# Performance work log

Measured on AMD Instinct MI355X. Metric: run time of the kernel, lower is better.

The kernel has to match this reference:

```python
import jax, jax.numpy as jnp
import numpy as np

B, T, N_EMBED, HEAD_SIZE = 8, 2048, 1024, 64


def setup_inputs() -> dict:
    key = jax.random.key(0)
    kx, kq, kk, kv = jax.random.split(key, 4)
    x = jax.random.normal(kx, (B, T, N_EMBED), dtype=jnp.float32)
    # nn.Linear(n_embed, head_size, bias=False) -> weight [head_size, n_embed];
    # we store the transposed [n_embed, head_size] so projection is x @ W.
    s = 1.0 / np.sqrt(N_EMBED)
    Wq = jax.random.normal(kq, (N_EMBED, HEAD_SIZE), dtype=jnp.float32) * s
    Wk = jax.random.normal(kk, (N_EMBED, HEAD_SIZE), dtype=jnp.float32) * s
    Wv = jax.random.normal(kv, (N_EMBED, HEAD_SIZE), dtype=jnp.float32) * s
    pad_mask = jnp.ones((B, T), dtype=jnp.int32)
    return {"x": x, "pad_mask": pad_mask, "Wq": Wq, "Wk": Wk, "Wv": Wv}


def reference(x, pad_mask, Wq, Wk, Wv):
    Bq, Tq, C = x.shape  # C == n_embed
    q = x @ Wq  # [B,T,H]
    k = x @ Wk  # self-attention path (enc_x is None)
    v = x @ Wv
    # NOTE: original divides by C**0.5 with C = n_embed, not head_size.
    scores = jnp.einsum("bth,bsh->bts", q, k) / jnp.sqrt(jnp.asarray(C, x.dtype))
    causal = jnp.tril(jnp.ones((Tq, Tq), dtype=bool))  # tril[:T,:T] != 0
    keep = causal[None, :, :] & (pad_mask[:, None, :] != 0)  # [B,T,T]
    scores = jnp.where(keep, scores, -jnp.inf)
    attn = jax.nn.softmax(scores, axis=-1)
    return jnp.einsum("bts,bsh->bth", attn, v)  # [B,T,head_size]
```

## Files before the change

### kernel.cpp

```cpp
#include <hip/hip_runtime.h>

#define DEV static __device__ __forceinline__

typedef float f32x4 __attribute__((ext_vector_type(4)));
typedef __bf16 bf16x8 __attribute__((ext_vector_type(8)));
typedef unsigned short u16x8 __attribute__((ext_vector_type(8)));
typedef unsigned short u16x4 __attribute__((ext_vector_type(4)));

#define MFMA(a, b, c) __builtin_amdgcn_mfma_f32_16x16x32_bf16((a), (b), (c), 0, 0, 0)

#define TT 2048
#define CE 1024
#define HS 64

#define WBT_E 0
#define Q_E   196608
#define K_E   (Q_E + 1048576)
#define VT_E  (K_E + 1048576)
#define PO_E  (VT_E + 1048576)
#define PML_E (PO_E + 2097152)
#define BIAS_E (PML_E + 131072)

DEV unsigned short cvt_bf16(float f) {
    unsigned int u = __builtin_bit_cast(unsigned int, f);
    u += 0x7FFFu + ((u >> 16) & 1u);
    return (unsigned short)(u >> 16);
}

DEV float bf2f(unsigned short v) {
    unsigned int u = ((unsigned int)v) << 16;
    return __builtin_bit_cast(float, u);
}

DEV bf16x8 ld_bf8(const unsigned short* p) {
    union { u16x8 u; bf16x8 b; } v;
    v.u = *(const u16x8*)p;
    return v.b;
}

DEV bf16x8 as_bf8(u16x8 u) {
    union { u16x8 u; bf16x8 b; } v;
    v.u = u;
    return v.b;
}

DEV void glds16(const void* g, void* l) {
    __builtin_amdgcn_global_load_lds(
        (const __attribute__((address_space(1))) void*)g,
        (__attribute__((address_space(3))) void*)l, 16, 0, 0);
}

__global__ __launch_bounds__(256) void wconv_kernel(
        const float* __restrict__ Wq, const float* __restrict__ Wk,
        const float* __restrict__ Wv, unsigned short* __restrict__ wbt) {
    __shared__ unsigned short Tr[64 * 72];
    const int blk = blockIdx.x;
    const int head = blk >> 4, kt = blk & 15;
    const int k0 = kt * 64;
    const float* W = (head == 0) ? Wq : ((head == 1) ? Wk : Wv);
    const float sc = (head == 0) ? 0.045084220027780106f : 1.0f;
    const int t = threadIdx.x;
    const int rrow = t >> 4, c4 = (t & 15) * 4;
    for (int i = 0; i < 4; ++i) {
        int krow = rrow + i * 16;
        f32x4 f = *(const f32x4*)(W + (size_t)(k0 + krow) * 64 + c4);
        Tr[(c4 + 0) * 72 + krow] = cvt_bf16(f[0] * sc);
        Tr[(c4 + 1) * 72 + krow] = cvt_bf16(f[1] * sc);
        Tr[(c4 + 2) * 72 + krow] = cvt_bf16(f[2] * sc);
        Tr[(c4 + 3) * 72 + krow] = cvt_bf16(f[3] * sc);
    }
    __syncthreads();
    const int n = t >> 2, off = (t & 3) * 16;
    u16x8 a0 = *(const u16x8*)&Tr[n * 72 + off];
    u16x8 a1 = *(const u16x8*)&Tr[n * 72 + off + 8];
    unsigned short* dst = wbt + head * 65536 + n * 1024 + k0 + off;
    *(u16x8*)dst = a0;
    *(u16x8*)(dst + 8) = a1;
}

__global__ __launch_bounds__(256) void bias_kernel(
        const int* __restrict__ pm, float* __restrict__ biasf) {
    int i = blockIdx.x * 256 + threadIdx.x;
    biasf[i] = pm[i] ? 0.0f : -1e30f;
}

__global__ __launch_bounds__(256) void proj_kernel(
        const float* __restrict__ x, const unsigned short* __restrict__ wbt,
        unsigned short* __restrict__ qws, unsigned short* __restrict__ kws,
        unsigned short* __restrict__ vtws) {
    __shared__ __align__(16) float Xt[2][1024];
    __shared__ __align__(16) unsigned short Wt[2][6144];
    __shared__ __align__(16) unsigned short TT2[64 * 48];

    const int t = threadIdx.x;
    const int lane = t & 63, w = t >> 6;
    const int quad = lane >> 4, c = lane & 15;
    const int wm = w & 1, wn = w >> 1;
    const int t0 = blockIdx.x * 32;

    const int srow = lane >> 3, scb = (lane & 7) ^ srow;
    const float* xg = x + (size_t)(t0 + w * 8 + srow) * CE + scb * 4;
    const int wrow_lo = lane >> 2;
    const int wcb = (lane & 3) ^ (wrow_lo & 3);
    const unsigned short* wg0 = wbt + (size_t)((3 * w + 0) * 16 + wrow_lo) * 1024 + wcb * 8;
    const unsigned short* wg1 = wbt + (size_t)((3 * w + 1) * 16 + wrow_lo) * 1024 + wcb * 8;
    const unsigned short* wg2 = wbt + (size_t)((3 * w + 2) * 16 + wrow_lo) * 1024 + wcb * 8;

    f32x4 acc[6] = {};

    glds16(xg, &Xt[0][w * 256]);
    glds16(wg0, &Wt[0][(3 * w + 0) * 512]);
    glds16(wg1, &Wt[0][(3 * w + 1) * 512]);
    glds16(wg2, &Wt[0][(3 * w + 2) * 512]);
    __syncthreads();

    const int r = wm * 16 + c;
    const int ck7 = c & 7, ck3 = c & 3;

    for (int step = 0; step < 32; ++step) {
        const int pb = step & 1, nb = pb ^ 1;
        const int ksn = ((step + 1) & 31) * 32;
        glds16(xg + ksn, &Xt[nb][w * 256]);
        glds16(wg0 + ksn, &Wt[nb][(3 * w + 0) * 512]);
        glds16(wg1 + ksn, &Wt[nb][(3 * w + 1) * 512]);
        glds16(wg2 + ksn, &Wt[nb][(3 * w + 2) * 512]);
        f32x4 v0 = *(const f32x4*)&Xt[pb][r * 32 + (((2 * quad) ^ ck7) * 4)];
        f32x4 v1 = *(const f32x4*)&Xt[pb][r * 32 + (((2 * quad + 1) ^ ck7) * 4)];
        u16x8 ap;
#pragma unroll
        for (int j = 0; j < 4; ++j) { ap[j] = cvt_bf16(v0[j]); ap[4 + j] = cvt_bf16(v1[j]); }
        bf16x8 af = as_bf8(ap);
#pragma unroll
        for (int nt = 0; nt < 6; ++nt) {
            int n = wn * 96 + nt * 16 + c;
            bf16x8 bb = ld_bf8(&Wt[pb][n * 32 + ((quad ^ ck3) * 8)]);
            acc[nt] = MFMA(af, bb, acc[nt]);
        }
        __syncthreads();
    }

    for (int nt = 0; nt < 6; ++nt) {
        int col = wn * 96 + nt * 16 + c;
        f32x4 a = acc[nt];
        for (int r4 = 0; r4 < 4; ++r4) {
            int row = wm * 16 + quad * 4 + r4;
            size_t tg = (size_t)(t0 + row);
            unsigned short hv = cvt_bf16(a[r4]);
            if (col < 64)       qws[tg * HS + col] = hv;
            else if (col < 128) kws[tg * HS + col - 64] = hv;
            else                TT2[(col - 128) * 48 + row] = hv;
        }
    }
    __syncthreads();
    {
        int h = t >> 2, off = (t & 3) * 8;
        u16x8 v = *(const u16x8*)&TT2[h * 48 + off];
        int b = t0 >> 11, tl0 = t0 & 2047;
        *(u16x8*)(vtws + (size_t)(b * 64 + h) * TT + tl0 + off) = v;
    }
}

__global__ __launch_bounds__(256) void flash_kernel(
        const unsigned short* __restrict__ qws, const unsigned short* __restrict__ kws,
        const unsigned short* __restrict__ vtws, const float* __restrict__ biasf,
        unsigned short* __restrict__ pO, float* __restrict__ pml) {
    __shared__ __align__(16) unsigned short Kt[2][4096];
    __shared__ __align__(16) unsigned short Vt[2][4096];
    __shared__ __align__(16) unsigned short Ps[4][1152];

    const int t = threadIdx.x, blk = blockIdx.x;
    const int sp = blk >> 8, r8 = blk & 255, b = r8 & 7;
    int qt = r8 >> 3;
    if (sp) qt = 31 - qt;
    if (sp && qt == 0) return;
    const int half = (qt + 2) >> 1;
    const int jbeg = sp ? half : 0;
    const int jend = sp ? qt + 1 : half;

    const int lane = t & 63, w = t >> 6;
    const int quad = lane >> 4, c = lane & 15;

    const int srow = lane >> 3, scb = (lane & 7) ^ srow;
    const unsigned short* kg0 = kws + (size_t)(b * TT + 2 * w * 8 + srow) * HS + scb * 8;
    const unsigned short* kg1 = kg0 + (size_t)8 * HS;
    const unsigned short* vg0 = vtws + (size_t)(b * 64 + 2 * w * 8 + srow) * TT + scb * 8;
    const unsigned short* vg1 = vg0 + (size_t)8 * TT;

    bf16x8 qf[2];
#pragma unroll
    for (int kk = 0; kk < 2; ++kk)
        qf[kk] = ld_bf8(qws + (size_t)(b * TT + qt * 64 + w * 16 + c) * HS + kk * 32 + quad * 8);

    const float* bbase = biasf + b * TT + quad * 4;
    const int ck7 = c & 7;

    {
        int kv = jbeg * 64;
        glds16(kg0 + (size_t)kv * HS, &Kt[0][(2 * w + 0) * 512]);
        glds16(kg1 + (size_t)kv * HS, &Kt[0][(2 * w + 1) * 512]);
        glds16(vg0 + kv, &Vt[0][(2 * w + 0) * 512]);
        glds16(vg1 + kv, &Vt[0][(2 * w + 1) * 512]);
    }
    __syncthreads();

    f32x4 o[4] = {};
    float m_run = -1e30f, l_run = 0.0f;

    for (int j = jbeg; j < jend; ++j) {
        const int pb = (j - jbeg) & 1, nb = pb ^ 1;
        const int jn = (j + 1 < jend) ? j + 1 : j;
        {
            int kv = jn * 64;
            glds16(kg0 + (size_t)kv * HS, &Kt[nb][(2 * w + 0) * 512]);
            glds16(kg1 + (size_t)kv * HS, &Kt[nb][(2 * w + 1) * 512]);
            glds16(vg0 + kv, &Vt[nb][(2 * w + 0) * 512]);
            glds16(vg1 + kv, &Vt[nb][(2 * w + 1) * 512]);
        }
        f32x4 bv[4];
#pragma unroll
        for (int nt = 0; nt < 4; ++nt)
            bv[nt] = *(const f32x4*)(bbase + j * 64 + nt * 16);

        f32x4 s4[4] = {};
#pragma unroll
        for (int kk = 0; kk < 2; ++kk)
#pragma unroll
            for (int nt = 0; nt < 4; ++nt) {
                bf16x8 ka = ld_bf8(&Kt[pb][(nt * 16 + c) * 64 + (((kk * 4 + quad) ^ ck7) * 8)]);
                s4[nt] = MFMA(ka, qf[kk], s4[nt]);
            }

        if (j == qt) {
            const int qrl = w * 16 + c;
#pragma unroll
            for (int nt = 0; nt < 4; ++nt)
#pragma unroll
                for (int r = 0; r < 4; ++r) {
                    int kvl = nt * 16 + quad * 4 + r;
                    s4[nt][r] = (kvl > qrl) ? -1e30f : (s4[nt][r] + bv[nt][r]);
                }
        } else {
#pragma unroll
            for (int nt = 0; nt < 4; ++nt)
#pragma unroll
                for (int r = 0; r < 4; ++r) s4[nt][r] += bv[nt][r];
        }

        float mx = s4[0][0];
#pragma unroll
        for (int nt = 0; nt < 4; ++nt)
#pragma unroll
            for (int r = 0; r < 4; ++r) mx = fmaxf(mx, s4[nt][r]);
        mx = fmaxf(mx, __shfl_xor(mx, 16, 64));
        mx = fmaxf(mx, __shfl_xor(mx, 32, 64));
        float mnew = fmaxf(m_run, mx);
        float al = exp2f(m_run - mnew);
        m_run = mnew;
#pragma unroll
        for (int nt = 0; nt < 4; ++nt)
#pragma unroll
            for (int r = 0; r < 4; ++r) s4[nt][r] = exp2f(s4[nt][r] - mnew);
        float rs = 0.0f;
#pragma unroll
        for (int nt = 0; nt < 4; ++nt)
            rs += (s4[nt][0] + s4[nt][1]) + (s4[nt][2] + s4[nt][3]);
        rs += __shfl_xor(rs, 16, 64);
        rs += __shfl_xor(rs, 32, 64);
        l_run = l_run * al + rs;
#pragma unroll
        for (int ht = 0; ht < 4; ++ht)
#pragma unroll
            for (int r = 0; r < 4; ++r) o[ht][r] *= al;

#pragma unroll
        for (int nt = 0; nt < 4; ++nt) {
            u16x4 pk;
#pragma unroll
            for (int r = 0; r < 4; ++r) pk[r] = cvt_bf16(s4[nt][r]);
            *(u16x4*)&Ps[w][c * 72 + nt * 16 + quad * 4] = pk;
        }
        bf16x8 p0 = ld_bf8(&Ps[w][c * 72 + quad * 8]);
        bf16x8 p1 = ld_bf8(&Ps[w][c * 72 + 32 + quad * 8]);

#pragma unroll
        for (int kk = 0; kk < 2; ++kk) {
            bf16x8 pa = kk ? p1 : p0;
#pragma unroll
            for (int ht = 0; ht < 4; ++ht) {
                bf16x8 va = ld_bf8(&Vt[pb][(ht * 16 + c) * 64 + (((kk * 4 + quad) ^ ck7) * 8)]);
                o[ht] = MFMA(va, pa, o[ht]);
            }
        }
        __syncthreads();
    }

    unsigned short* po = pO + (size_t)blk * 4096;
#pragma unroll
    for (int ht = 0; ht < 4; ++ht) {
        u16x4 pk;
#pragma unroll
        for (int r = 0; r < 4; ++r) pk[r] = cvt_bf16(o[ht][r]);
        *(u16x4*)(po + (w * 16 + c) * 64 + ht * 16 + quad * 4) = pk;
    }
    if (quad == 0) {
        pml[(size_t)blk * 128 + (w * 16 + c) * 2] = m_run;
        pml[(size_t)blk * 128 + (w * 16 + c) * 2 + 1] = l_run;
    }
}

__global__ __launch_bounds__(256) void combine_kernel(
        const unsigned short* __restrict__ pO, const float* __restrict__ pml,
        float* __restrict__ out) {
    const int blk = blockIdx.x;
    const int qt = blk >> 3, b = blk & 7;
    const int s0 = qt * 8 + b, s1 = 256 + (31 - qt) * 8 + b;
    const bool two = (qt > 0);
    const int t = threadIdx.x, h = t & 63, rg = t >> 6;
    for (int i = 0; i < 16; ++i) {
        int row = rg + i * 4;
        float m0 = pml[(size_t)s0 * 128 + row * 2];
        float l0 = pml[(size_t)s0 * 128 + row * 2 + 1];
        float o0 = bf2f(pO[(size_t)s0 * 4096 + row * 64 + h]);
        float num, den;
        if (two) {
            float m1 = pml[(size_t)s1 * 128 + row * 2];
            float l1 = pml[(size_t)s1 * 128 + row * 2 + 1];
            float o1 = bf2f(pO[(size_t)s1 * 4096 + row * 64 + h]);
            float M = fmaxf(m0, m1);
            float w0 = exp2f(m0 - M), w1 = exp2f(m1 - M);
            num = o0 * w0 + o1 * w1;
            den = l0 * w0 + l1 * w1;
        } else {
            num = o0; den = l0;
        }
        out[(size_t)(b * TT + qt * 64 + row) * HS + h] = num / den;
    }
}

extern "C" void kernel_launch(void* const* d_in, const int* in_sizes, int n_in,
                              void* d_out, int out_size, void* d_ws, size_t ws_size,
                              hipStream_t stream) {
    const float* x  = (const float*)d_in[0];
    const int* pm   = (const int*)d_in[1];
    const float* Wq = (const float*)d_in[2];
    const float* Wk = (const float*)d_in[3];
    const float* Wv = (const float*)d_in[4];
    float* out = (float*)d_out;

    unsigned short* wsu  = (unsigned short*)d_ws;
    unsigned short* wbt  = wsu + WBT_E;
    unsigned short* qws  = wsu + Q_E;
    unsigned short* kws  = wsu + K_E;
    unsigned short* vtws = wsu + VT_E;
    unsigned short* pO   = wsu + PO_E;
    float* pml           = (float*)(wsu + PML_E);
    float* biasf         = (float*)(wsu + BIAS_E);

    wconv_kernel<<<48, 256, 0, stream>>>(Wq, Wk, Wv, wbt);
    bias_kernel<<<64, 256, 0, stream>>>(pm, biasf);
    proj_kernel<<<512, 256, 0, stream>>>(x, wbt, qws, kws, vtws);
    flash_kernel<<<512, 256, 0, stream>>>(qws, kws, vtws, biasf, pO, pml);
    combine_kernel<<<256, 256, 0, stream>>>(pO, pml, out);
}
```

Baseline: 168.0 us.

## Triple-buffer LDS loads with partial vmcnt waits in projection and flash kernels

Both the projection GEMM and the flash-attention loop move from double to triple buffering of global-to-LDS tiles. A single barrier preceded by s_waitcnt vmcnt(4) replaces the trailing __syncthreads, so the loads for tile i+2 can stay in flight while tile i is computed. The flash kernel also stages the padding bias for its key range into LDS once up front instead of reading it from global memory every iteration. This costs more LDS per block, which may reduce occupancy, and it depends on the hand-set vmcnt count matching the exact number of outstanding loads.

```diff
diff --git a/kernel.cpp b/kernel.cpp
--- a/kernel.cpp
+++ b/kernel.cpp
@@ -8,6 +8,8 @@
 typedef unsigned short u16x4 __attribute__((ext_vector_type(4)));
 
 #define MFMA(a, b, c) __builtin_amdgcn_mfma_f32_16x16x32_bf16((a), (b), (c), 0, 0, 0)
+
+#define WAIT4_BARRIER() asm volatile("s_waitcnt vmcnt(4)\n\ts_barrier" ::: "memory")
 
 #define TT 2048
 #define CE 1024
@@ -88,8 +90,8 @@
         const float* __restrict__ x, const unsigned short* __restrict__ wbt,
         unsigned short* __restrict__ qws, unsigned short* __restrict__ kws,
         unsigned short* __restrict__ vtws) {
-    __shared__ __align__(16) float Xt[2][1024];
-    __shared__ __align__(16) unsigned short Wt[2][6144];
+    __shared__ __align__(16) float Xt[3][1024];
+    __shared__ __align__(16) unsigned short Wt[3][6144];
     __shared__ __align__(16) unsigned short TT2[64 * 48];
 
     const int t = threadIdx.x;
@@ -108,35 +110,40 @@
 
     f32x4 acc[6] = {};
 
-    glds16(xg, &Xt[0][w * 256]);
-    glds16(wg0, &Wt[0][(3 * w + 0) * 512]);
-    glds16(wg1, &Wt[0][(3 * w + 1) * 512]);
-    glds16(wg2, &Wt[0][(3 * w + 2) * 512]);
-    __syncthreads();
+#pragma unroll
+    for (int s = 0; s < 2; ++s) {
+        const int ks = s * 32;
+        glds16(xg + ks, &Xt[s][w * 256]);
+        glds16(wg0 + ks, &Wt[s][(3 * w + 0) * 512]);
+        glds16(wg1 + ks, &Wt[s][(3 * w + 1) * 512]);
+        glds16(wg2 + ks, &Wt[s][(3 * w + 2) * 512]);
+    }
 
     const int r = wm * 16 + c;
     const int ck7 = c & 7, ck3 = c & 3;
 
+    int pb = 0, nb = 2;
     for (int step = 0; step < 32; ++step) {
-        const int pb = step & 1, nb = pb ^ 1;
-        const int ksn = ((step + 1) & 31) * 32;
+        WAIT4_BARRIER();
+        f32x4 v0 = *(const f32x4*)&Xt[pb][r * 32 + (((2 * quad) ^ ck7) * 4)];
+        f32x4 v1 = *(const f32x4*)&Xt[pb][r * 32 + (((2 * quad + 1) ^ ck7) * 4)];
+        u16x8 ap;
+#pragma unroll
+        for (int j = 0; j < 4; ++j) { ap[j] = cvt_bf16(v0[j]); ap[4 + j] = cvt_bf16(v1[j]); }
+        bf16x8 af = as_bf8(ap);
+#pragma unroll
+        for (int nt = 0; nt < 6; ++nt) {
+            int n = wn * 96 + nt * 16 + c;
+            bf16x8 bb = ld_bf8(&Wt[pb][n * 32 + ((quad ^ ck3) * 8)]);
+            acc[nt] = MFMA(af, bb, acc[nt]);
+        }
+        const int ksn = ((step + 2) & 31) * 32;
         glds16(xg + ksn, &Xt[nb][w * 256]);
         glds16(wg0 + ksn, &Wt[nb][(3 * w + 0) * 512]);
         glds16(wg1 + ksn, &Wt[nb][(3 * w + 1) * 512]);
         glds16(wg2 + ksn, &Wt[nb][(3 * w + 2) * 512]);
-        f32x4 v0 = *(const f32x4*)&Xt[pb][r * 32 + (((2 * quad) ^ ck7) * 4)];
-        f32x4 v1 = *(const f32x4*)&Xt[pb][r * 32 + (((2 * quad + 1) ^ ck7) * 4)];
-        u16x8 ap;
-#pragma unroll
-        for (int j = 0; j < 4; ++j) { ap[j] = cvt_bf16(v0[j]); ap[4 + j] = cvt_bf16(v1[j]); }
-        bf16x8 af = as_bf8(ap);
-#pragma unroll
-        for (int nt = 0; nt < 6; ++nt) {
-            int n = wn * 96 + nt * 16 + c;
-            bf16x8 bb = ld_bf8(&Wt[pb][n * 32 + ((quad ^ ck3) * 8)]);
-            acc[nt] = MFMA(af, bb, acc[nt]);
-        }
-        __syncthreads();
+        pb = (pb == 2) ? 0 : pb + 1;
+        nb = (nb == 2) ? 0 : nb + 1;
     }
 
     for (int nt = 0; nt < 6; ++nt) {
@@ -164,9 +171,10 @@
         const unsigned short* __restrict__ qws, const unsigned short* __restrict__ kws,
         const unsigned short* __restrict__ vtws, const float* __restrict__ biasf,
         unsigned short* __restrict__ pO, float* __restrict__ pml) {
-    __shared__ __align__(16) unsigned short Kt[2][4096];
-    __shared__ __align__(16) unsigned short Vt[2][4096];
+    __shared__ __align__(16) unsigned short Kt[3][4096];
+    __shared__ __align__(16) unsigned short Vt[3][4096];
     __shared__ __align__(16) unsigned short Ps[4][1152];
+    __shared__ __align__(16) float Bs[1024];
 
     const int t = threadIdx.x, blk = blockIdx.x;
     const int sp = blk >> 8, r8 = blk & 255, b = r8 & 7;
@@ -176,6 +184,7 @@
     const int half = (qt + 2) >> 1;
     const int jbeg = sp ? half : 0;
     const int jend = sp ? qt + 1 : half;
+    const int niter = jend - jbeg;
 
     const int lane = t & 63, w = t >> 6;
     const int quad = lane >> 4, c = lane & 15;
@@ -191,35 +200,34 @@
     for (int kk = 0; kk < 2; ++kk)
         qf[kk] = ld_bf8(qws + (size_t)(b * TT + qt * 64 + w * 16 + c) * HS + kk * 32 + quad * 8);
 
-    const float* bbase = biasf + b * TT + quad * 4;
-    const int ck7 = c & 7;
-
     {
-        int kv = jbeg * 64;
-        glds16(kg0 + (size_t)kv * HS, &Kt[0][(2 * w + 0) * 512]);
-        glds16(kg1 + (size_t)kv * HS, &Kt[0][(2 * w + 1) * 512]);
-        glds16(vg0 + kv, &Vt[0][(2 * w + 0) * 512]);
-        glds16(vg1 + kv, &Vt[0][(2 * w + 1) * 512]);
+        int bi = t * 4;
+        if (bi < niter * 64)
+            *(f32x4*)&Bs[bi] = *(const f32x4*)(biasf + b * TT + jbeg * 64 + bi);
+    }
+
+#pragma unroll
+    for (int s = 0; s < 2; ++s) {
+        int jj = jbeg + s; if (jj > jend - 1) jj = jend - 1;
+        const int kv = jj * 64;
+        glds16(kg0 + (size_t)kv * HS, &Kt[s][(2 * w + 0) * 512]);
+        glds16(kg1 + (size_t)kv * HS, &Kt[s][(2 * w + 1) * 512]);
+        glds16(vg0 + kv, &Vt[s][(2 * w + 0) * 512]);
+        glds16(vg1 + kv, &Vt[s][(2 * w + 1) * 512]);
     }
     __syncthreads();
 
     f32x4 o[4] = {};
     float m_run = -1e30f, l_run = 0.0f;
-
+    const int ck7 = c & 7;
+
+    int pb = 0, nb = 2;
     for (int j = jbeg; j < jend; ++j) {
-        const int pb = (j - jbeg) & 1, nb = pb ^ 1;
-        const int jn = (j + 1 < jend) ? j + 1 : j;
-        {
-            int kv = jn * 64;
-            glds16(kg0 + (size_t)kv * HS, &Kt[nb][(2 * w + 0) * 512]);
-            glds16(kg1 + (size_t)kv * HS, &Kt[nb][(2 * w + 1) * 512]);
-            glds16(vg0 + kv, &Vt[nb][(2 * w + 0) * 512]);
-            glds16(vg1 + kv, &Vt[nb][(2 * w + 1) * 512]);
-        }
+        WAIT4_BARRIER();
         f32x4 bv[4];
 #pragma unroll
         for (int nt = 0; nt < 4; ++nt)
-            bv[nt] = *(const f32x4*)(bbase + j * 64 + nt * 16);
+            bv[nt] = *(const f32x4*)&Bs[(j - jbeg) * 64 + nt * 16 + quad * 4];
 
         f32x4 s4[4] = {};
 #pragma unroll
@@ -291,7 +299,17 @@
                 o[ht] = MFMA(va, pa, o[ht]);
             }
         }
-        __syncthreads();
+
+        {
+            int jn = j + 2; if (jn > jend - 1) jn = jend - 1;
+            const int kv = jn * 64;
+            glds16(kg0 + (size_t)kv * HS, &Kt[nb][(2 * w + 0) * 512]);
+            glds16(kg1 + (size_t)kv * HS, &Kt[nb][(2 * w + 1) * 512]);
+            glds16(vg0 + kv, &Vt[nb][(2 * w + 0) * 512]);
+            glds16(vg1 + kv, &Vt[nb][(2 * w + 1) * 512]);
+        }
+        pb = (pb == 2) ? 0 : pb + 1;
+        nb = (nb == 2) ? 0 : nb + 1;
     }
 
     unsigned short* po = pO + (size_t)blk * 4096;
```

Result: faster. 159.1 us (-5.3%).

## Deepen proj and flash pipelines to 4-stage LDS ring with vmcnt waits

Applied to the files above, without the earlier changes.

Replaces the double-buffered LDS staging in both the projection and flash kernels with a 4-buffer ring. Three stages are prefetched ahead, and each iteration uses an explicit s_waitcnt vmcnt(8) plus s_barrier instead of a full __syncthreads, so global-to-LDS loads overlap more compute. It also drops the separate bias kernel and builds the pad-mask bias in LDS inside the flash kernel. The costs are more LDS per block, which may lower occupancy, and fragile hand-counted waitcnt logic.

```diff
diff --git a/kernel.cpp b/kernel.cpp
--- a/kernel.cpp
+++ b/kernel.cpp
@@ -3,11 +3,16 @@
 #define DEV static __device__ __forceinline__
 
 typedef float f32x4 __attribute__((ext_vector_type(4)));
+typedef int i32x4 __attribute__((ext_vector_type(4)));
 typedef __bf16 bf16x8 __attribute__((ext_vector_type(8)));
 typedef unsigned short u16x8 __attribute__((ext_vector_type(8)));
 typedef unsigned short u16x4 __attribute__((ext_vector_type(4)));
 
 #define MFMA(a, b, c) __builtin_amdgcn_mfma_f32_16x16x32_bf16((a), (b), (c), 0, 0, 0)
+
+#define WAIT8_BARRIER() asm volatile("s_waitcnt vmcnt(8)\n\ts_barrier" ::: "memory")
+#define LGKM_BARRIER()  asm volatile("s_waitcnt lgkmcnt(0)\n\ts_barrier" ::: "memory")
+#define VM_DRAIN()      asm volatile("s_waitcnt vmcnt(0)" ::: "memory")
 
 #define TT 2048
 #define CE 1024
@@ -19,7 +24,6 @@
 #define VT_E  (K_E + 1048576)
 #define PO_E  (VT_E + 1048576)
 #define PML_E (PO_E + 2097152)
-#define BIAS_E (PML_E + 131072)
 
 DEV unsigned short cvt_bf16(float f) {
     unsigned int u = __builtin_bit_cast(unsigned int, f);
@@ -78,18 +82,12 @@
     *(u16x8*)(dst + 8) = a1;
 }
 
-__global__ __launch_bounds__(256) void bias_kernel(
-        const int* __restrict__ pm, float* __restrict__ biasf) {
-    int i = blockIdx.x * 256 + threadIdx.x;
-    biasf[i] = pm[i] ? 0.0f : -1e30f;
-}
-
 __global__ __launch_bounds__(256) void proj_kernel(
         const float* __restrict__ x, const unsigned short* __restrict__ wbt,
         unsigned short* __restrict__ qws, unsigned short* __restrict__ kws,
         unsigned short* __restrict__ vtws) {
-    __shared__ __align__(16) float Xt[2][1024];
-    __shared__ __align__(16) unsigned short Wt[2][6144];
+    __shared__ __align__(16) float Xt0[1024], Xt1[1024], Xt2[1024], Xt3[1024];
+    __shared__ __align__(16) unsigned short Wt0[6144], Wt1[6144], Wt2[6144], Wt3[6144];
     __shared__ __align__(16) unsigned short TT2[64 * 48];
 
     const int t = threadIdx.x;
@@ -106,38 +104,43 @@
     const unsigned short* wg1 = wbt + (size_t)((3 * w + 1) * 16 + wrow_lo) * 1024 + wcb * 8;
     const unsigned short* wg2 = wbt + (size_t)((3 * w + 2) * 16 + wrow_lo) * 1024 + wcb * 8;
 
+#define PSTAGE(XD, WD, ksn) \
+    glds16(xg + (ksn), &XD[w * 256]); \
+    glds16(wg0 + (ksn), &WD[(3 * w + 0) * 512]); \
+    glds16(wg1 + (ksn), &WD[(3 * w + 1) * 512]); \
+    glds16(wg2 + (ksn), &WD[(3 * w + 2) * 512]);
+
     f32x4 acc[6] = {};
 
-    glds16(xg, &Xt[0][w * 256]);
-    glds16(wg0, &Wt[0][(3 * w + 0) * 512]);
-    glds16(wg1, &Wt[0][(3 * w + 1) * 512]);
-    glds16(wg2, &Wt[0][(3 * w + 2) * 512]);
-    __syncthreads();
+    PSTAGE(Xt0, Wt0, 0)
+    PSTAGE(Xt1, Wt1, 32)
+    PSTAGE(Xt2, Wt2, 64)
 
     const int r = wm * 16 + c;
     const int ck7 = c & 7, ck3 = c & 3;
 
-    for (int step = 0; step < 32; ++step) {
-        const int pb = step & 1, nb = pb ^ 1;
-        const int ksn = ((step + 1) & 31) * 32;
-        glds16(xg + ksn, &Xt[nb][w * 256]);
-        glds16(wg0 + ksn, &Wt[nb][(3 * w + 0) * 512]);
-        glds16(wg1 + ksn, &Wt[nb][(3 * w + 1) * 512]);
-        glds16(wg2 + ksn, &Wt[nb][(3 * w + 2) * 512]);
-        f32x4 v0 = *(const f32x4*)&Xt[pb][r * 32 + (((2 * quad) ^ ck7) * 4)];
-        f32x4 v1 = *(const f32x4*)&Xt[pb][r * 32 + (((2 * quad + 1) ^ ck7) * 4)];
-        u16x8 ap;
-#pragma unroll
-        for (int j = 0; j < 4; ++j) { ap[j] = cvt_bf16(v0[j]); ap[4 + j] = cvt_bf16(v1[j]); }
-        bf16x8 af = as_bf8(ap);
-#pragma unroll
-        for (int nt = 0; nt < 6; ++nt) {
-            int n = wn * 96 + nt * 16 + c;
-            bf16x8 bb = ld_bf8(&Wt[pb][n * 32 + ((quad ^ ck3) * 8)]);
-            acc[nt] = MFMA(af, bb, acc[nt]);
-        }
-        __syncthreads();
-    }
+#define PITER(step, XT, WT, XD, WD) { \
+    WAIT8_BARRIER(); \
+    f32x4 v0 = *(const f32x4*)&XT[r * 32 + (((2 * quad) ^ ck7) * 4)]; \
+    f32x4 v1 = *(const f32x4*)&XT[r * 32 + (((2 * quad + 1) ^ ck7) * 4)]; \
+    u16x8 ap; \
+    _Pragma("unroll") for (int j = 0; j < 4; ++j) { \
+        ap[j] = cvt_bf16(v0[j]); ap[4 + j] = cvt_bf16(v1[j]); } \
+    bf16x8 af = as_bf8(ap); \
+    _Pragma("unroll") for (int nt = 0; nt < 6; ++nt) { \
+        bf16x8 bb = ld_bf8(&WT[(wn * 96 + nt * 16 + c) * 32 + ((quad ^ ck3) * 8)]); \
+        acc[nt] = MFMA(af, bb, acc[nt]); } \
+    const int ksn = (((step) + 3) & 31) * 32; \
+    PSTAGE(XD, WD, ksn) }
+
+    for (int s = 0; s < 32; s += 4) {
+        PITER(s + 0, Xt0, Wt0, Xt3, Wt3)
+        PITER(s + 1, Xt1, Wt1, Xt0, Wt0)
+        PITER(s + 2, Xt2, Wt2, Xt1, Wt1)
+        PITER(s + 3, Xt3, Wt3, Xt2, Wt2)
+    }
+#undef PITER
+#undef PSTAGE
 
     for (int nt = 0; nt < 6; ++nt) {
         int col = wn * 96 + nt * 16 + c;
@@ -162,11 +165,12 @@
 
 __global__ __launch_bounds__(256) void flash_kernel(
         const unsigned short* __restrict__ qws, const unsigned short* __restrict__ kws,
-        const unsigned short* __restrict__ vtws, const float* __restrict__ biasf,
+        const unsigned short* __restrict__ vtws, const int* __restrict__ pmask,
         unsigned short* __restrict__ pO, float* __restrict__ pml) {
-    __shared__ __align__(16) unsigned short Kt[2][4096];
-    __shared__ __align__(16) unsigned short Vt[2][4096];
+    __shared__ __align__(16) unsigned short Kt0[4096], Kt1[4096], Kt2[4096], Kt3[4096];
+    __shared__ __align__(16) unsigned short Vt0[4096], Vt1[4096], Vt2[4096], Vt3[4096];
     __shared__ __align__(16) unsigned short Ps[4][1152];
+    __shared__ __align__(16) float Bs[1024];
 
     const int t = threadIdx.x, blk = blockIdx.x;
     const int sp = blk >> 8, r8 = blk & 255, b = r8 & 7;
@@ -176,6 +180,7 @@
     const int half = (qt + 2) >> 1;
     const int jbeg = sp ? half : 0;
     const int jend = sp ? qt + 1 : half;
+    const int niter = jend - jbeg;
 
     const int lane = t & 63, w = t >> 6;
     const int quad = lane >> 4, c = lane & 15;
@@ -186,113 +191,105 @@
     const unsigned short* vg0 = vtws + (size_t)(b * 64 + 2 * w * 8 + srow) * TT + scb * 8;
     const unsigned short* vg1 = vg0 + (size_t)8 * TT;
 
+#define FSTAGE(KD, VD, kv) \
+    glds16(kg0 + (size_t)(kv) * HS, &KD[(2 * w + 0) * 512]); \
+    glds16(kg1 + (size_t)(kv) * HS, &KD[(2 * w + 1) * 512]); \
+    glds16(vg0 + (kv), &VD[(2 * w + 0) * 512]); \
+    glds16(vg1 + (kv), &VD[(2 * w + 1) * 512]);
+
     bf16x8 qf[2];
 #pragma unroll
     for (int kk = 0; kk < 2; ++kk)
         qf[kk] = ld_bf8(qws + (size_t)(b * TT + qt * 64 + w * 16 + c) * HS + kk * 32 + quad * 8);
 
-    const float* bbase = biasf + b * TT + quad * 4;
-    const int ck7 = c & 7;
-
     {
-        int kv = jbeg * 64;
-        glds16(kg0 + (size_t)kv * HS, &Kt[0][(2 * w + 0) * 512]);
-        glds16(kg1 + (size_t)kv * HS, &Kt[0][(2 * w + 1) * 512]);
-        glds16(vg0 + kv, &Vt[0][(2 * w + 0) * 512]);
-        glds16(vg1 + kv, &Vt[0][(2 * w + 1) * 512]);
-    }
-    __syncthreads();
+        int bi = t * 4;
+        if (bi < niter * 64) {
+            i32x4 pmv = *(const i32x4*)(pmask + b * TT + jbeg * 64 + bi);
+            f32x4 bvv;
+#pragma unroll
+            for (int j = 0; j < 4; ++j) bvv[j] = pmv[j] ? 0.0f : -1e30f;
+            *(f32x4*)&Bs[bi] = bvv;
+        }
+    }
+
+    {
+        int j1 = (jbeg + 1 > jend - 1) ? jend - 1 : jbeg + 1;
+        int j2 = (jbeg + 2 > jend - 1) ? jend - 1 : jbeg + 2;
+        FSTAGE(Kt0, Vt0, jbeg * 64)
+        FSTAGE(Kt1, Vt1, j1 * 64)
+        FSTAGE(Kt2, Vt2, j2 * 64)
+    }
+    LGKM_BARRIER();
 
     f32x4 o[4] = {};
     float m_run = -1e30f, l_run = 0.0f;
-
-    for (int j = jbeg; j < jend; ++j) {
-        const int pb = (j - jbeg) & 1, nb = pb ^ 1;
-        const int jn = (j + 1 < jend) ? j + 1 : j;
-        {
-            int kv = jn * 64;
-            glds16(kg0 + (size_t)kv * HS, &Kt[nb][(2 * w + 0) * 512]);
-            glds16(kg1 + (size_t)kv * HS, &Kt[nb][(2 * w + 1) * 512]);
-            glds16(vg0 + kv, &Vt[nb][(2 * w + 0) * 512]);
-            glds16(vg1 + kv, &Vt[nb][(2 * w + 1) * 512]);
-        }
-        f32x4 bv[4];
-#pragma unroll
-        for (int nt = 0; nt < 4; ++nt)
-            bv[nt] = *(const f32x4*)(bbase + j * 64 + nt * 16);
-
-        f32x4 s4[4] = {};
-#pragma unroll
-        for (int kk = 0; kk < 2; ++kk)
-#pragma unroll
-            for (int nt = 0; nt < 4; ++nt) {
-                bf16x8 ka = ld_bf8(&Kt[pb][(nt * 16 + c) * 64 + (((kk * 4 + quad) ^ ck7) * 8)]);
-                s4[nt] = MFMA(ka, qf[kk], s4[nt]);
-            }
-
-        if (j == qt) {
-            const int qrl = w * 16 + c;
-#pragma unroll
-            for (int nt = 0; nt < 4; ++nt)
-#pragma unroll
-                for (int r = 0; r < 4; ++r) {
-                    int kvl = nt * 16 + quad * 4 + r;
-                    s4[nt][r] = (kvl > qrl) ? -1e30f : (s4[nt][r] + bv[nt][r]);
-                }
-        } else {
-#pragma unroll
-            for (int nt = 0; nt < 4; ++nt)
-#pragma unroll
-                for (int r = 0; r < 4; ++r) s4[nt][r] += bv[nt][r];
-        }
-
-        float mx = s4[0][0];
-#pragma unroll
-        for (int nt = 0; nt < 4; ++nt)
-#pragma unroll
-            for (int r = 0; r < 4; ++r) mx = fmaxf(mx, s4[nt][r]);
-        mx = fmaxf(mx, __shfl_xor(mx, 16, 64));
-        mx = fmaxf(mx, __shfl_xor(mx, 32, 64));
-        float mnew = fmaxf(m_run, mx);
-        float al = exp2f(m_run - mnew);
-        m_run = mnew;
-#pragma unroll
-        for (int nt = 0; nt < 4; ++nt)
-#pragma unroll
-            for (int r = 0; r < 4; ++r) s4[nt][r] = exp2f(s4[nt][r] - mnew);
-        float rs = 0.0f;
-#pragma unroll
-        for (int nt = 0; nt < 4; ++nt)
-            rs += (s4[nt][0] + s4[nt][1]) + (s4[nt][2] + s4[nt][3]);
-        rs += __shfl_xor(rs, 16, 64);
-        rs += __shfl_xor(rs, 32, 64);
-        l_run = l_run * al + rs;
-#pragma unroll
-        for (int ht = 0; ht < 4; ++ht)
-#pragma unroll
-            for (int r = 0; r < 4; ++r) o[ht][r] *= al;
-
-#pragma unroll
-        for (int nt = 0; nt < 4; ++nt) {
-            u16x4 pk;
-#pragma unroll
-            for (int r = 0; r < 4; ++r) pk[r] = cvt_bf16(s4[nt][r]);
-            *(u16x4*)&Ps[w][c * 72 + nt * 16 + quad * 4] = pk;
-        }
-        bf16x8 p0 = ld_bf8(&Ps[w][c * 72 + quad * 8]);
-        bf16x8 p1 = ld_bf8(&Ps[w][c * 72 + 32 + quad * 8]);
-
-#pragma unroll
-        for (int kk = 0; kk < 2; ++kk) {
-            bf16x8 pa = kk ? p1 : p0;
-#pragma unroll
-            for (int ht = 0; ht < 4; ++ht) {
-                bf16x8 va = ld_bf8(&Vt[pb][(ht * 16 + c) * 64 + (((kk * 4 + quad) ^ ck7) * 8)]);
-                o[ht] = MFMA(va, pa, o[ht]);
-            }
-        }
-        __syncthreads();
-    }
+    const int ck7 = c & 7;
+
+#define FITER(u, KT, VT, KD, VD) \
+    if (j0 + (u) < jend) { \
+        const int j = j0 + (u); \
+        WAIT8_BARRIER(); \
+        f32x4 bv[4]; \
+        _Pragma("unroll") for (int nt = 0; nt < 4; ++nt) \
+            bv[nt] = *(const f32x4*)&Bs[(j - jbeg) * 64 + nt * 16 + quad * 4]; \
+        f32x4 s4[4] = {}; \
+        _Pragma("unroll") for (int kk = 0; kk < 2; ++kk) \
+        _Pragma("unroll") for (int nt = 0; nt < 4; ++nt) { \
+            bf16x8 ka = ld_bf8(&KT[(nt * 16 + c) * 64 + (((kk * 4 + quad) ^ ck7) * 8)]); \
+            s4[nt] = MFMA(ka, qf[kk], s4[nt]); } \
+        if (j == qt) { \
+            const int qrl = w * 16 + c; \
+            _Pragma("unroll") for (int nt = 0; nt < 4; ++nt) \
+            _Pragma("unroll") for (int r = 0; r < 4; ++r) { \
+                int kvl = nt * 16 + quad * 4 + r; \
+                s4[nt][r] = (kvl > qrl) ? -1e30f : (s4[nt][r] + bv[nt][r]); } \
+        } else { \
+            _Pragma("unroll") for (int nt = 0; nt < 4; ++nt) \
+            _Pragma("unroll") for (int r = 0; r < 4; ++r) s4[nt][r] += bv[nt][r]; } \
+        float mx = s4[0][0]; \
+        _Pragma("unroll") for (int nt = 0; nt < 4; ++nt) \
+        _Pragma("unroll") for (int r = 0; r < 4; ++r) mx = fmaxf(mx, s4[nt][r]); \
+        mx = fmaxf(mx, __shfl_xor(mx, 16, 64)); \
+        mx = fmaxf(mx, __shfl_xor(mx, 32, 64)); \
+        float mnew = fmaxf(m_run, mx); \
+        float al = exp2f(m_run - mnew); \
+        m_run = mnew; \
+        _Pragma("unroll") for (int nt = 0; nt < 4; ++nt) \
+        _Pragma("unroll") for (int r = 0; r < 4; ++r) s4[nt][r] = exp2f(s4[nt][r] - mnew); \
+        float rs = 0.0f; \
+        _Pragma("unroll") for (int nt = 0; nt < 4; ++nt) \
+            rs += (s4[nt][0] + s4[nt][1]) + (s4[nt][2] + s4[nt][3]); \
+        rs += __shfl_xor(rs, 16, 64); \
+        rs += __shfl_xor(rs, 32, 64); \
+        l_run = l_run * al + rs; \
+        _Pragma("unroll") for (int ht = 0; ht < 4; ++ht) \
+        _Pragma("unroll") for (int r = 0; r < 4; ++r) o[ht][r] *= al; \
+        _Pragma("unroll") for (int nt = 0; nt < 4; ++nt) { \
+            u16x4 pk; \
+            _Pragma("unroll") for (int r = 0; r < 4; ++r) pk[r] = cvt_bf16(s4[nt][r]); \
+            *(u16x4*)&Ps[w][c * 72 + nt * 16 + quad * 4] = pk; } \
+        bf16x8 p0 = ld_bf8(&Ps[w][c * 72 + quad * 8]); \
+        bf16x8 p1 = ld_bf8(&Ps[w][c * 72 + 32 + quad * 8]); \
+        _Pragma("unroll") for (int kk = 0; kk < 2; ++kk) { \
+            bf16x8 pa = kk ? p1 : p0; \
+            _Pragma("unroll") for (int ht = 0; ht < 4; ++ht) { \
+                bf16x8 va = ld_bf8(&VT[(ht * 16 + c) * 64 + (((kk * 4 + quad) ^ ck7) * 8)]); \
+                o[ht] = MFMA(va, pa, o[ht]); } } \
+        int jn = j + 3; if (jn > jend - 1) jn = jend - 1; \
+        FSTAGE(KD, VD, jn * 64) \
+    }
+
+    for (int j0 = jbeg; j0 < jend; j0 += 4) {
+        FITER(0, Kt0, Vt0, Kt3, Vt3)
+        FITER(1, Kt1, Vt1, Kt0, Vt0)
+        FITER(2, Kt2, Vt2, Kt1, Vt1)
+        FITER(3, Kt3, Vt3, Kt2, Vt2)
+    }
+#undef FITER
+#undef FSTAGE
+
+    VM_DRAIN();
 
     unsigned short* po = pO + (size_t)blk * 4096;
 #pragma unroll
@@ -354,11 +351,9 @@
     unsigned short* vtws = wsu + VT_E;
     unsigned short* pO   = wsu + PO_E;
     float* pml           = (float*)(wsu + PML_E);
-    float* biasf         = (float*)(wsu + BIAS_E);
 
     wconv_kernel<<<48, 256, 0, stream>>>(Wq, Wk, Wv, wbt);
-    bias_kernel<<<64, 256, 0, stream>>>(pm, biasf);
     proj_kernel<<<512, 256, 0, stream>>>(x, wbt, qws, kws, vtws);
-    flash_kernel<<<512, 256, 0, stream>>>(qws, kws, vtws, biasf, pO, pml);
+    flash_kernel<<<512, 256, 0, stream>>>(qws, kws, vtws, pm, pO, pml);
     combine_kernel<<<256, 256, 0, stream>>>(pO, pml, out);
 }
```

After: 158.4 us. 1.06x faster.

## Replace LDS staging with direct register prefetch in projection and flash kernels

Applied to the files above, without the earlier changes.

Projection and flash kernels stop staging X, W, K and V tiles through shared memory with global_load_lds and block barriers. Each lane now loads its MFMA operand fragments straight from global memory into registers, with one- or two-step software prefetch. The separate bias kernel is dropped and the pad mask is read directly inside the flash kernel. This removes LDS traffic, __syncthreads and one launch, but waves that share a tile now load overlapping data redundantly through cache, and register pressure rises (launch bounds now request two blocks per SM).

```diff
diff --git a/kernel.cpp b/kernel.cpp
--- a/kernel.cpp
+++ b/kernel.cpp
@@ -3,6 +3,7 @@
 #define DEV static __device__ __forceinline__
 
 typedef float f32x4 __attribute__((ext_vector_type(4)));
+typedef int i32x4 __attribute__((ext_vector_type(4)));
 typedef __bf16 bf16x8 __attribute__((ext_vector_type(8)));
 typedef unsigned short u16x8 __attribute__((ext_vector_type(8)));
 typedef unsigned short u16x4 __attribute__((ext_vector_type(4)));
@@ -19,7 +20,6 @@
 #define VT_E  (K_E + 1048576)
 #define PO_E  (VT_E + 1048576)
 #define PML_E (PO_E + 2097152)
-#define BIAS_E (PML_E + 131072)
 
 DEV unsigned short cvt_bf16(float f) {
     unsigned int u = __builtin_bit_cast(unsigned int, f);
@@ -42,12 +42,6 @@
     union { u16x8 u; bf16x8 b; } v;
     v.u = u;
     return v.b;
-}
-
-DEV void glds16(const void* g, void* l) {
-    __builtin_amdgcn_global_load_lds(
-        (const __attribute__((address_space(1))) void*)g,
-        (__attribute__((address_space(3))) void*)l, 16, 0, 0);
 }
 
 __global__ __launch_bounds__(256) void wconv_kernel(
@@ -78,18 +72,10 @@
     *(u16x8*)(dst + 8) = a1;
 }
 
-__global__ __launch_bounds__(256) void bias_kernel(
-        const int* __restrict__ pm, float* __restrict__ biasf) {
-    int i = blockIdx.x * 256 + threadIdx.x;
-    biasf[i] = pm[i] ? 0.0f : -1e30f;
-}
-
-__global__ __launch_bounds__(256) void proj_kernel(
+__global__ __launch_bounds__(256, 2) void proj_kernel(
         const float* __restrict__ x, const unsigned short* __restrict__ wbt,
         unsigned short* __restrict__ qws, unsigned short* __restrict__ kws,
         unsigned short* __restrict__ vtws) {
-    __shared__ __align__(16) float Xt[2][1024];
-    __shared__ __align__(16) unsigned short Wt[2][6144];
     __shared__ __align__(16) unsigned short TT2[64 * 48];
 
     const int t = threadIdx.x;
@@ -98,45 +84,40 @@
     const int wm = w & 1, wn = w >> 1;
     const int t0 = blockIdx.x * 32;
 
-    const int srow = lane >> 3, scb = (lane & 7) ^ srow;
-    const float* xg = x + (size_t)(t0 + w * 8 + srow) * CE + scb * 4;
-    const int wrow_lo = lane >> 2;
-    const int wcb = (lane & 3) ^ (wrow_lo & 3);
-    const unsigned short* wg0 = wbt + (size_t)((3 * w + 0) * 16 + wrow_lo) * 1024 + wcb * 8;
-    const unsigned short* wg1 = wbt + (size_t)((3 * w + 1) * 16 + wrow_lo) * 1024 + wcb * 8;
-    const unsigned short* wg2 = wbt + (size_t)((3 * w + 2) * 16 + wrow_lo) * 1024 + wcb * 8;
+    const float* xg = x + (size_t)(t0 + wm * 16 + c) * CE + quad * 8;
+    const unsigned short* wg = wbt + (size_t)(wn * 96 + c) * 1024 + quad * 8;
 
     f32x4 acc[6] = {};
-
-    glds16(xg, &Xt[0][w * 256]);
-    glds16(wg0, &Wt[0][(3 * w + 0) * 512]);
-    glds16(wg1, &Wt[0][(3 * w + 1) * 512]);
-    glds16(wg2, &Wt[0][(3 * w + 2) * 512]);
-    __syncthreads();
-
-    const int r = wm * 16 + c;
-    const int ck7 = c & 7, ck3 = c & 3;
+    f32x4 x0a, x0b, x1a, x1b;
+    u16x8 w0[6];
+
+    x0a = *(const f32x4*)(xg);
+    x0b = *(const f32x4*)(xg + 4);
+    x1a = *(const f32x4*)(xg + 32);
+    x1b = *(const f32x4*)(xg + 36);
+#pragma unroll
+    for (int nt = 0; nt < 6; ++nt)
+        w0[nt] = *(const u16x8*)(wg + nt * 16384);
 
     for (int step = 0; step < 32; ++step) {
-        const int pb = step & 1, nb = pb ^ 1;
-        const int ksn = ((step + 1) & 31) * 32;
-        glds16(xg + ksn, &Xt[nb][w * 256]);
-        glds16(wg0 + ksn, &Wt[nb][(3 * w + 0) * 512]);
-        glds16(wg1 + ksn, &Wt[nb][(3 * w + 1) * 512]);
-        glds16(wg2 + ksn, &Wt[nb][(3 * w + 2) * 512]);
-        f32x4 v0 = *(const f32x4*)&Xt[pb][r * 32 + (((2 * quad) ^ ck7) * 4)];
-        f32x4 v1 = *(const f32x4*)&Xt[pb][r * 32 + (((2 * quad + 1) ^ ck7) * 4)];
+        const int ksW = ((step + 1) & 31) * 32;
+        const int ksX = ((step + 2) & 31) * 32;
+        u16x8 w1[6];
+#pragma unroll
+        for (int nt = 0; nt < 6; ++nt)
+            w1[nt] = *(const u16x8*)(wg + nt * 16384 + ksW);
+        f32x4 x2a = *(const f32x4*)(xg + ksX);
+        f32x4 x2b = *(const f32x4*)(xg + ksX + 4);
         u16x8 ap;
 #pragma unroll
-        for (int j = 0; j < 4; ++j) { ap[j] = cvt_bf16(v0[j]); ap[4 + j] = cvt_bf16(v1[j]); }
+        for (int j = 0; j < 4; ++j) { ap[j] = cvt_bf16(x0a[j]); ap[4 + j] = cvt_bf16(x0b[j]); }
         bf16x8 af = as_bf8(ap);
 #pragma unroll
-        for (int nt = 0; nt < 6; ++nt) {
-            int n = wn * 96 + nt * 16 + c;
-            bf16x8 bb = ld_bf8(&Wt[pb][n * 32 + ((quad ^ ck3) * 8)]);
-            acc[nt] = MFMA(af, bb, acc[nt]);
-        }
-        __syncthreads();
+        for (int nt = 0; nt < 6; ++nt)
+            acc[nt] = MFMA(af, as_bf8(w0[nt]), acc[nt]);
+        x0a = x1a; x0b = x1b; x1a = x2a; x1b = x2b;
+#pragma unroll
+        for (int nt = 0; nt < 6; ++nt) w0[nt] = w1[nt];
     }
 
     for (int nt = 0; nt < 6; ++nt) {
@@ -160,17 +141,15 @@
     }
 }
 
-__global__ __launch_bounds__(256) void flash_kernel(
+__global__ __launch_bounds__(256, 2) void flash_kernel(
         const unsigned short* __restrict__ qws, const unsigned short* __restrict__ kws,
-        const unsigned short* __restrict__ vtws, const float* __restrict__ biasf,
+        const unsigned short* __restrict__ vtws, const int* __restrict__ pmask,
         unsigned short* __restrict__ pO, float* __restrict__ pml) {
-    __shared__ __align__(16) unsigned short Kt[2][4096];
-    __shared__ __align__(16) unsigned short Vt[2][4096];
     __shared__ __align__(16) unsigned short Ps[4][1152];
 
     const int t = threadIdx.x, blk = blockIdx.x;
-    const int sp = blk >> 8, r8 = blk & 255, b = r8 & 7;
-    int qt = r8 >> 3;
+    const int sp = blk >> 8, r8i = blk & 255, b = r8i & 7;
+    int qt = r8i >> 3;
     if (sp) qt = 31 - qt;
     if (sp && qt == 0) return;
     const int half = (qt + 2) >> 1;
@@ -180,55 +159,54 @@
     const int lane = t & 63, w = t >> 6;
     const int quad = lane >> 4, c = lane & 15;
 
-    const int srow = lane >> 3, scb = (lane & 7) ^ srow;
-    const unsigned short* kg0 = kws + (size_t)(b * TT + 2 * w * 8 + srow) * HS + scb * 8;
-    const unsigned short* kg1 = kg0 + (size_t)8 * HS;
-    const unsigned short* vg0 = vtws + (size_t)(b * 64 + 2 * w * 8 + srow) * TT + scb * 8;
-    const unsigned short* vg1 = vg0 + (size_t)8 * TT;
+    const unsigned short* kbase = kws + (size_t)(b * TT + c) * HS + quad * 8;
+    const unsigned short* vbase = vtws + (size_t)(b * 64 + c) * TT + quad * 8;
+    const int* pmb = pmask + b * TT + quad * 4;
 
     bf16x8 qf[2];
 #pragma unroll
     for (int kk = 0; kk < 2; ++kk)
         qf[kk] = ld_bf8(qws + (size_t)(b * TT + qt * 64 + w * 16 + c) * HS + kk * 32 + quad * 8);
 
-    const float* bbase = biasf + b * TT + quad * 4;
-    const int ck7 = c & 7;
-
-    {
-        int kv = jbeg * 64;
-        glds16(kg0 + (size_t)kv * HS, &Kt[0][(2 * w + 0) * 512]);
-        glds16(kg1 + (size_t)kv * HS, &Kt[0][(2 * w + 1) * 512]);
-        glds16(vg0 + kv, &Vt[0][(2 * w + 0) * 512]);
-        glds16(vg1 + kv, &Vt[0][(2 * w + 1) * 512]);
-    }
-    __syncthreads();
+    u16x8 kc[4][2];
+#pragma unroll
+    for (int nt = 0; nt < 4; ++nt)
+#pragma unroll
+        for (int kk = 0; kk < 2; ++kk)
+            kc[nt][kk] = *(const u16x8*)(kbase + (size_t)(jbeg * 64 + nt * 16) * HS + kk * 32);
 
     f32x4 o[4] = {};
     float m_run = -1e30f, l_run = 0.0f;
 
     for (int j = jbeg; j < jend; ++j) {
-        const int pb = (j - jbeg) & 1, nb = pb ^ 1;
-        const int jn = (j + 1 < jend) ? j + 1 : j;
+        const int kv0 = j * 64;
+        i32x4 pmv[4];
+#pragma unroll
+        for (int nt = 0; nt < 4; ++nt)
+            pmv[nt] = *(const i32x4*)(pmb + kv0 + nt * 16);
+        u16x8 vc[4][2];
+#pragma unroll
+        for (int ht = 0; ht < 4; ++ht)
+#pragma unroll
+            for (int kx = 0; kx < 2; ++kx)
+                vc[ht][kx] = *(const u16x8*)(vbase + (size_t)(ht * 16) * TT + kv0 + kx * 32);
+
+        f32x4 s4[4] = {};
+#pragma unroll
+        for (int kk = 0; kk < 2; ++kk)
+#pragma unroll
+            for (int nt = 0; nt < 4; ++nt)
+                s4[nt] = MFMA(as_bf8(kc[nt][kk]), qf[kk], s4[nt]);
+
+        u16x8 kn[4][2];
         {
-            int kv = jn * 64;
-            glds16(kg0 + (size_t)kv * HS, &Kt[nb][(2 * w + 0) * 512]);
-            glds16(kg1 + (size_t)kv * HS, &Kt[nb][(2 * w + 1) * 512]);
-            glds16(vg0 + kv, &Vt[nb][(2 * w + 0) * 512]);
-            glds16(vg1 + kv, &Vt[nb][(2 * w + 1) * 512]);
-        }
-        f32x4 bv[4];
-#pragma unroll
-        for (int nt = 0; nt < 4; ++nt)
-            bv[nt] = *(const f32x4*)(bbase + j * 64 + nt * 16);
-
-        f32x4 s4[4] = {};
-#pragma unroll
-        for (int kk = 0; kk < 2; ++kk)
-#pragma unroll
-            for (int nt = 0; nt < 4; ++nt) {
-                bf16x8 ka = ld_bf8(&Kt[pb][(nt * 16 + c) * 64 + (((kk * 4 + quad) ^ ck7) * 8)]);
-                s4[nt] = MFMA(ka, qf[kk], s4[nt]);
-            }
+            int jn = (j + 1 < jend) ? j + 1 : j;
+#pragma unroll
+            for (int nt = 0; nt < 4; ++nt)
+#pragma unroll
+                for (int kk = 0; kk < 2; ++kk)
+                    kn[nt][kk] = *(const u16x8*)(kbase + (size_t)(jn * 64 + nt * 16) * HS + kk * 32);
+        }
 
         if (j == qt) {
             const int qrl = w * 16 + c;
@@ -237,13 +215,15 @@
 #pragma unroll
                 for (int r = 0; r < 4; ++r) {
                     int kvl = nt * 16 + quad * 4 + r;
-                    s4[nt][r] = (kvl > qrl) ? -1e30f : (s4[nt][r] + bv[nt][r]);
+                    bool dead = (kvl > qrl) || (pmv[nt][r] == 0);
+                    s4[nt][r] = dead ? -1e30f : s4[nt][r];
                 }
         } else {
 #pragma unroll
             for (int nt = 0; nt < 4; ++nt)
 #pragma unroll
-                for (int r = 0; r < 4; ++r) s4[nt][r] += bv[nt][r];
+                for (int r = 0; r < 4; ++r)
+                    s4[nt][r] = (pmv[nt][r] == 0) ? -1e30f : s4[nt][r];
         }
 
         float mx = s4[0][0];
@@ -283,15 +263,15 @@
         bf16x8 p1 = ld_bf8(&Ps[w][c * 72 + 32 + quad * 8]);
 
 #pragma unroll
-        for (int kk = 0; kk < 2; ++kk) {
-            bf16x8 pa = kk ? p1 : p0;
-#pragma unroll
-            for (int ht = 0; ht < 4; ++ht) {
-                bf16x8 va = ld_bf8(&Vt[pb][(ht * 16 + c) * 64 + (((kk * 4 + quad) ^ ck7) * 8)]);
-                o[ht] = MFMA(va, pa, o[ht]);
-            }
-        }
-        __syncthreads();
+        for (int ht = 0; ht < 4; ++ht) {
+            o[ht] = MFMA(as_bf8(vc[ht][0]), p0, o[ht]);
+            o[ht] = MFMA(as_bf8(vc[ht][1]), p1, o[ht]);
+        }
+
+#pragma unroll
+        for (int nt = 0; nt < 4; ++nt)
+#pragma unroll
+            for (int kk = 0; kk < 2; ++kk) kc[nt][kk] = kn[nt][kk];
     }
 
     unsigned short* po = pO + (size_t)blk * 4096;
@@ -354,11 +334,9 @@
     unsigned short* vtws = wsu + VT_E;
     unsigned short* pO   = wsu + PO_E;
     float* pml           = (float*)(wsu + PML_E);
-    float* biasf         = (float*)(wsu + BIAS_E);
 
     wconv_kernel<<<48, 256, 0, stream>>>(Wq, Wk, Wv, wbt);
-    bias_kernel<<<64, 256, 0, stream>>>(pm, biasf);
     proj_kernel<<<512, 256, 0, stream>>>(x, wbt, qws, kws, vtws);
-    flash_kernel<<<512, 256, 0, stream>>>(qws, kws, vtws, biasf, pO, pml);
+    flash_kernel<<<512, 256, 0, stream>>>(qws, kws, vtws, pm, pO, pml);
     combine_kernel<<<256, 256, 0, stream>>>(pO, pml, out);
 }
```

Result: slower. 203.8 us (+21.3%).
